# Kernel optimization log

Hardware: AMD Instinct MI355X
Metric: run time of the kernel (lower is better)

Reference implementation:

```python
import jax, jax.numpy as jnp
import numpy as np

D_MODEL = 2048
D_INNER = 4096            # expand * d_model
D_XB = 1024
D_STATE = 128
HEADDIM = 64
NHEADS = D_INNER // HEADDIM            # 64
NGROUPS = D_INNER // D_STATE           # 32 (d_inner == ngroups * d_state)
HPG = NHEADS // NGROUPS                # heads per B/C group = 2
REPEAT = D_INNER // D_XB               # repeat_kv factor = 4
XB_GROUPS = D_XB // D_STATE            # 8
CHUNK = 256
D_CONV = 4
CONV_DIM = D_INNER + 2 * D_XB          # 6144
D_IN_PROJ = D_INNER + 2 * D_XB + D_INNER + NHEADS  # 10304 -> d_mlp = 0
NORM_GS = D_INNER // NGROUPS           # gated group-RMSNorm group size = 128
EPS = 1e-5


def setup_inputs() -> dict:
    key = jax.random.key(0)
    ks = jax.random.split(key, 8)
    u = jax.random.normal(ks[0], (2, 2048, D_MODEL), jnp.float32)
    W_in = jax.random.normal(ks[1], (D_IN_PROJ, D_MODEL), jnp.float32) * 0.02
    conv_w = jax.random.normal(ks[2], (CONV_DIM, D_CONV), jnp.float32) * 0.2
    conv_b = jnp.zeros((CONV_DIM,), jnp.float32)
    # dt_bias = inverse-softplus of dt ~ LogUniform(dt_min, dt_max), as in __init__
    dt = jnp.exp(jax.random.uniform(ks[3], (NHEADS,), jnp.float32)
                 * (np.log(0.1) - np.log(0.001)) + np.log(0.001))
    dt_bias = dt + jnp.log(-jnp.expm1(-dt))
    A_log = jnp.log(jax.random.uniform(ks[4], (NHEADS,), jnp.float32, minval=1.0, maxval=16.0))
    D = jnp.ones((NHEADS,), jnp.float32)
    norm_weight = jnp.ones((D_INNER,), jnp.float32)
    W_out = jax.random.normal(ks[5], (D_MODEL, D_INNER), jnp.float32) * 0.02
    return dict(u=u, W_in=W_in, conv_w=conv_w, conv_b=conv_b, dt_bias=dt_bias,
                A_log=A_log, D=D, norm_weight=norm_weight, W_out=W_out)


def _segsum(x):
    # x: (..., T); out[..., t, s] = sum_{s < i <= t} x_i for s <= t else -inf
    T = x.shape[-1]
    cs = jnp.cumsum(x, axis=-1)
    seg = cs[..., :, None] - cs[..., None, :]
    mask = jnp.tril(jnp.ones((T, T), bool))
    return jnp.where(mask, seg, -jnp.inf)


def _chunked_scan(x, dt, A, Bh, Ch, D):
    # SSD chunked selective scan (mamba_chunk_scan_combined math).
    # x: (b,l,h,p), dt: (b,l,h) post-softplus, A: (h,), Bh/Ch: (b,l,h,n), D: (h,)
    b, l, h, p = x.shape
    c = l // CHUNK
    xc = x.reshape(b, c, CHUNK, h, p)
    dtc = dt.reshape(b, c, CHUNK, h)
    Bc = Bh.reshape(b, c, CHUNK, h, D_STATE)
    Cc = Ch.reshape(b, c, CHUNK, h, D_STATE)
    dA = jnp.transpose(dtc * A, (0, 3, 1, 2))          # (b,h,c,cl)
    dA_cs = jnp.cumsum(dA, axis=-1)                     # (b,h,c,cl)
    L = jnp.exp(_segsum(dA))                            # (b,h,c,cl,cl), lower-tri decay
    xdt = xc * dtc[..., None]                           # (b,c,cl,h,p)
    # intra-chunk (diagonal block) output
    G = jnp.einsum('bclhn,bcshn->bhcls', Cc, Bc)
    Y_diag = jnp.einsum('bhcls,bcshp->bclhp', G * L, xdt)
    # per-chunk final states
    decay_states = jnp.exp(dA_cs[..., -1:] - dA_cs)     # (b,h,c,cl)
    states = jnp.einsum('bcshn,bhcs,bcshp->bchpn', Bc, decay_states, xdt)
    # inter-chunk recurrence
    chunk_decay = jnp.exp(dA_cs[..., -1])               # (b,h,c)
    states_t = jnp.moveaxis(states, 1, 0)               # (c,b,h,p,n)
    decay_t = jnp.moveaxis(chunk_decay, -1, 0)          # (c,b,h)
    def step(carry, inp):
        s, d = inp
        return carry * d[..., None, None] + s, carry
    _, prev = jax.lax.scan(step, jnp.zeros_like(states_t[0]), (states_t, decay_t))
    prev = jnp.moveaxis(prev, 0, 1)                     # (b,c,h,p,n) state entering each chunk
    Y_off = jnp.einsum('bclhn,bchpn,bhcl->bclhp', Cc, prev, jnp.exp(dA_cs))
    y = Y_diag + Y_off + xc * D[:, None]                # D skip uses raw x
    return y.reshape(b, l, h, p)


def reference(u, W_in, conv_w, conv_b, dt_bias, A_log, D, norm_weight, W_out):
    b, l, _ = u.shape
    zxbcdt = u @ W_in.T                                 # (b,l,10304); d_mlp == 0
    z, xBC, dt = jnp.split(zxbcdt, [D_INNER, D_INNER + CONV_DIM], axis=-1)
    # causal depthwise conv1d (kernel D_CONV) + SiLU (causal_conv1d_fn semantics)
    xp = jnp.pad(xBC, ((0, 0), (D_CONV - 1, 0), (0, 0)))
    conv = conv_b
    for k in range(D_CONV):
        conv = conv + xp[:, k:k + l, :] * conv_w[:, k]
    xBC = jax.nn.silu(conv)
    x, B, C = jnp.split(xBC, [D_XB, 2 * D_XB], axis=-1)
    # GQA-style repeat_kv (repeat_interleave over d_state-sized groups)
    x = jnp.repeat(x.reshape(b, l, XB_GROUPS, D_STATE), REPEAT, axis=2).reshape(b, l, D_INNER)
    B = jnp.repeat(B.reshape(b, l, XB_GROUPS, D_STATE), REPEAT, axis=2)   # (b,l,NGROUPS,n)
    C = C.reshape(b, l, NGROUPS, D_STATE)
    # broadcast groups to heads (head h uses group h // HPG)
    Bh = jnp.repeat(B, HPG, axis=2)
    Ch = jnp.repeat(C, HPG, axis=2)
    xh = x.reshape(b, l, NHEADS, HEADDIM)
    dt = jax.nn.softplus(dt + dt_bias)                  # dt_softplus=True
    A = -jnp.exp(A_log)
    y = _chunked_scan(xh, dt, A, Bh, Ch, D).reshape(b, l, D_INNER)
    # RMSNormGated (norm_before_gate=False): gate then grouped RMSNorm
    y = y * jax.nn.silu(z)
    yg = y.reshape(b, l, NGROUPS, NORM_GS)
    rstd = jax.lax.rsqrt(jnp.mean(yg * yg, axis=-1, keepdims=True) + EPS)
    y = (yg * rstd).reshape(b, l, D_INNER) * norm_weight
    return y @ W_out.T
```

## Files before the change

kernel.cpp:

```cpp
#include <hip/hip_runtime.h>
#include <cstdint>
#include <cstddef>

typedef unsigned int uint;
typedef unsigned short ushort;

typedef __bf16 bf16x8 __attribute__((ext_vector_type(8)));
typedef float f32x4 __attribute__((ext_vector_type(4)));

__device__ __forceinline__ float bflo(uint u) { return __uint_as_float(u << 16); }
__device__ __forceinline__ float bfhi(uint u) { return __uint_as_float(u & 0xffff0000u); }
__device__ __forceinline__ float bf2f(ushort s) { return __uint_as_float(((uint)s) << 16); }
__device__ __forceinline__ ushort f2bf(float f) {
    uint u = __float_as_uint(f);
    u += 0x7fffu + ((u >> 16) & 1u);
    return (ushort)(u >> 16);
}
__device__ __forceinline__ uint pk2(float lo, float hi) {
    return (uint)f2bf(lo) | ((uint)f2bf(hi) << 16);
}
__device__ __forceinline__ void unpack8(uint4 v, float* f) {
    f[0] = bflo(v.x); f[1] = bfhi(v.x); f[2] = bflo(v.y); f[3] = bfhi(v.y);
    f[4] = bflo(v.z); f[5] = bfhi(v.z); f[6] = bflo(v.w); f[7] = bfhi(v.w);
}

typedef __attribute__((address_space(1))) const unsigned int* as1_cuptr;
typedef __attribute__((address_space(3))) unsigned int* as3_uptr;
__device__ __forceinline__ void gload_lds16(const void* g, void* l) {
    __builtin_amdgcn_global_load_lds((as1_cuptr)g, (as3_uptr)l, 16, 0, 0);
}

#define LTOT 4096
#define DMODEL 2048
#define DINNER 4096
#define DSTATE 128
#define NHEADS 64
#define CONVDIM 6144
#define DPROJ 10304
#define CHUNK 256
#define NCHUNK 16

__global__ void cvt_kernel(const float* __restrict__ in, ushort* __restrict__ out, int n4) {
    int i = blockIdx.x * 256 + threadIdx.x;
    if (i < n4) {
        float4 v = ((const float4*)in)[i];
        ushort4 o;
        o.x = f2bf(v.x); o.y = f2bf(v.y); o.z = f2bf(v.z); o.w = f2bf(v.w);
        ((ushort4*)out)[i] = o;
    }
}

#define MFMA_OP __builtin_amdgcn_mfma_f32_16x16x32_bf16
#define MM16(MB) do { \
  acc[(MB)+0][0]=MFMA_OP(a0,b0,acc[(MB)+0][0],0,0,0); acc[(MB)+0][1]=MFMA_OP(a0,b1,acc[(MB)+0][1],0,0,0); \
  acc[(MB)+0][2]=MFMA_OP(a0,b2,acc[(MB)+0][2],0,0,0); acc[(MB)+0][3]=MFMA_OP(a0,b3,acc[(MB)+0][3],0,0,0); \
  acc[(MB)+1][0]=MFMA_OP(a1,b0,acc[(MB)+1][0],0,0,0); acc[(MB)+1][1]=MFMA_OP(a1,b1,acc[(MB)+1][1],0,0,0); \
  acc[(MB)+1][2]=MFMA_OP(a1,b2,acc[(MB)+1][2],0,0,0); acc[(MB)+1][3]=MFMA_OP(a1,b3,acc[(MB)+1][3],0,0,0); \
  acc[(MB)+2][0]=MFMA_OP(a2,b0,acc[(MB)+2][0],0,0,0); acc[(MB)+2][1]=MFMA_OP(a2,b1,acc[(MB)+2][1],0,0,0); \
  acc[(MB)+2][2]=MFMA_OP(a2,b2,acc[(MB)+2][2],0,0,0); acc[(MB)+2][3]=MFMA_OP(a2,b3,acc[(MB)+2][3],0,0,0); \
  acc[(MB)+3][0]=MFMA_OP(a3,b0,acc[(MB)+3][0],0,0,0); acc[(MB)+3][1]=MFMA_OP(a3,b1,acc[(MB)+3][1],0,0,0); \
  acc[(MB)+3][2]=MFMA_OP(a3,b2,acc[(MB)+3][2],0,0,0); acc[(MB)+3][3]=MFMA_OP(a3,b3,acc[(MB)+3][3],0,0,0); \
} while (0)

#define RD8(BASE, OFF) (*(const bf16x8*)((BASE) + (OFF)))

__global__ __launch_bounds__(512, 2) void gemm256_in(
    const ushort* __restrict__ X, const ushort* __restrict__ W,
    ushort* __restrict__ zbuf, ushort* __restrict__ xbc, float* __restrict__ dtraw) {
    __shared__ ushort AL[2][16384];
    __shared__ ushort BL[2][16384];
    const int NBN = 41;
    int q = gridDim.x >> 3;
    int wg = blockIdx.x;
    int swz = (wg & 7) * q + (wg >> 3);
    int per = NBN * 4;
    int sg = swz / per, rr = swz % per;
    int bm = sg * 4 + (rr & 3);
    int bn = rr >> 2;
    int tid = threadIdx.x;
    int lane = tid & 63, w = tid >> 6;
    int wr = w >> 2, wc = w & 3;
    int lr = lane & 15, g = lane >> 4;
    int y00 = ((lr >> 1) << 7) | ((lr & 1) << 6) | (g << 4);
    int z00 = y00 ^ (((y00 >> 7) & 7) << 4);
    int aBase = wr * 8192 + z00;
    int bBase = wc * 4096 + z00;
    int z0 = tid * 16, z1 = z0 + 8192;
    int y0 = z0 ^ (((z0 >> 7) & 7) << 4);
    int y1 = z1 ^ (((z1 >> 7) & 7) << 4);
    int row0s = ((y0 >> 7) << 1) | ((y0 >> 6) & 1), kbe0 = (y0 & 63) >> 1;
    int row1s = ((y1 >> 7) << 1) | ((y1 >> 6) & 1), kbe1 = (y1 & 63) >> 1;
    const ushort* gA0 = &X[(size_t)(bm * 256 + row0s) * 2048 + kbe0];
    const ushort* gA1 = &X[(size_t)(bm * 256 + row1s) * 2048 + kbe1];
    const ushort* gB0 = &W[(size_t)(bn * 256 + row0s) * 2048 + kbe0];
    const ushort* gB1 = &W[(size_t)(bn * 256 + row1s) * 2048 + kbe1];
    int wOff = w * 1024;

#define STAGE(DB, ARR, KP, P0, P1, KO) do { \
    gload_lds16((P0) + (KO) + (KP) * 32, (char*)(ARR) + (DB) * 32768 + (KP) * 16384 + wOff); \
    gload_lds16((P1) + (KO) + (KP) * 32, (char*)(ARR) + (DB) * 32768 + (KP) * 16384 + wOff + 8192); \
} while (0)

    f32x4 acc[8][4] = {};
    STAGE(0, AL, 0, gA0, gA1, 0);
    STAGE(0, BL, 0, gB0, gB1, 0);
    STAGE(0, AL, 1, gA0, gA1, 0);
    STAGE(0, BL, 1, gB0, gB1, 0);

    for (int t = 0; t < 32; ++t) {
        int buf = t & 1, nb = buf ^ 1;
        int ko = ((t + 1) & 31) * 64;
        const char* Ab = (const char*)AL + buf * 32768;
        const char* Bb = (const char*)BL + buf * 32768;
        bf16x8 a0, a1, a2, a3, b0, b1, b2, b3;
        asm volatile("s_waitcnt vmcnt(4)" ::: "memory");
        __builtin_amdgcn_s_barrier();
        __builtin_amdgcn_sched_barrier(0);
        b0 = RD8(Bb, bBase);        b1 = RD8(Bb, bBase + 1024);
        b2 = RD8(Bb, bBase + 2048); b3 = RD8(Bb, bBase + 3072);
        a0 = RD8(Ab, aBase);        a1 = RD8(Ab, aBase + 1024);
        a2 = RD8(Ab, aBase + 2048); a3 = RD8(Ab, aBase + 3072);
        STAGE(nb, AL, 0, gA0, gA1, ko);
        __builtin_amdgcn_s_setprio(1);
        MM16(0);
        __builtin_amdgcn_s_setprio(0);
        __builtin_amdgcn_sched_barrier(0);
        __builtin_amdgcn_s_barrier();
        __builtin_amdgcn_sched_barrier(0);
        a0 = RD8(Ab, aBase + 4096);        a1 = RD8(Ab, aBase + 4096 + 1024);
        a2 = RD8(Ab, aBase + 4096 + 2048); a3 = RD8(Ab, aBase + 4096 + 3072);
        STAGE(nb, BL, 0, gB0, gB1, ko);
        __builtin_amdgcn_s_setprio(1);
        MM16(4);
        __builtin_amdgcn_s_setprio(0);
        asm volatile("s_waitcnt vmcnt(4)" ::: "memory");
        __builtin_amdgcn_s_barrier();
        __builtin_amdgcn_sched_barrier(0);
        b0 = RD8(Bb, bBase + 16384);        b1 = RD8(Bb, bBase + 16384 + 1024);
        b2 = RD8(Bb, bBase + 16384 + 2048); b3 = RD8(Bb, bBase + 16384 + 3072);
        a0 = RD8(Ab, aBase + 16384);        a1 = RD8(Ab, aBase + 16384 + 1024);
        a2 = RD8(Ab, aBase + 16384 + 2048); a3 = RD8(Ab, aBase + 16384 + 3072);
        STAGE(nb, AL, 1, gA0, gA1, ko);
        __builtin_amdgcn_s_setprio(1);
        MM16(0);
        __builtin_amdgcn_s_setprio(0);
        __builtin_amdgcn_sched_barrier(0);
        __builtin_amdgcn_s_barrier();
        __builtin_amdgcn_sched_barrier(0);
        a0 = RD8(Ab, aBase + 16384 + 4096);        a1 = RD8(Ab, aBase + 16384 + 4096 + 1024);
        a2 = RD8(Ab, aBase + 16384 + 4096 + 2048); a3 = RD8(Ab, aBase + 16384 + 4096 + 3072);
        STAGE(nb, BL, 1, gB0, gB1, ko);
        __builtin_amdgcn_s_setprio(1);
        MM16(4);
        __builtin_amdgcn_s_setprio(0);
    }
    asm volatile("s_waitcnt vmcnt(0)" ::: "memory");

    int rq = g * 4;
    #pragma unroll
    for (int mf = 0; mf < 8; mf++) {
        int row0 = bm * 256 + wr * 128 + mf * 16 + rq;
        #pragma unroll
        for (int n = 0; n < 4; n++) {
            int cb0 = bn * 256 + wc * 64 + n * 16;
            int col = cb0 + lr;
            if (cb0 < 4096) {
                #pragma unroll
                for (int r = 0; r < 4; r++)
                    zbuf[(size_t)(row0 + r) * DINNER + col] = f2bf(acc[mf][n][r]);
            } else if (cb0 < 10240) {
                #pragma unroll
                for (int r = 0; r < 4; r++)
                    xbc[(size_t)(row0 + r) * CONVDIM + (col - 4096)] = f2bf(acc[mf][n][r]);
            } else if (cb0 < 10304) {
                #pragma unroll
                for (int r = 0; r < 4; r++)
                    dtraw[(size_t)(row0 + r) * 64 + (col - 10240)] = acc[mf][n][r];
            }
        }
    }
}
#undef STAGE

__global__ __launch_bounds__(256) void gemm_bf16_out(
    const ushort* __restrict__ X, const ushort* __restrict__ W,
    float* __restrict__ outF, int M, int N, int K, int NB) {
    __shared__ ushort As[128 * 32];
    __shared__ ushort Bs[128 * 32];
    int q = gridDim.x >> 3;
    int wg = blockIdx.x;
    int swz = (wg & 7) * q + (wg >> 3);
    int per = NB * 4;
    int sg = swz / per, rr = swz % per;
    int bm = sg * 4 + (rr & 3);
    int bn = rr >> 2;
    int tid = threadIdx.x;
    int lane = tid & 63, w = tid >> 6;
    int wr = w >> 1, wc = w & 1;
    int lr = lane & 15, lk = (lane >> 4) * 8;
    int r0 = lane >> 2;
    int ce = (lane & 3) * 8;
    const ushort* gA0 = &X[(size_t)(bm * 128 + (w * 2 + 0) * 16 + r0) * K + ce];
    const ushort* gA1 = &X[(size_t)(bm * 128 + (w * 2 + 1) * 16 + r0) * K + ce];
    const ushort* gB0 = &W[(size_t)(bn * 128 + (w * 2 + 0) * 16 + r0) * K + ce];
    const ushort* gB1 = &W[(size_t)(bn * 128 + (w * 2 + 1) * 16 + r0) * K + ce];
    ushort* lA0 = &As[(w * 2 + 0) * 512];
    ushort* lA1 = &As[(w * 2 + 1) * 512];
    ushort* lB0 = &Bs[(w * 2 + 0) * 512];
    ushort* lB1 = &Bs[(w * 2 + 1) * 512];
    f32x4 acc[4][4] = {};
    for (int kk = 0; kk < K; kk += 32) {
        __syncthreads();
        gload_lds16(gA0, lA0); gload_lds16(gA1, lA1);
        gload_lds16(gB0, lB0); gload_lds16(gB1, lB1);
        gA0 += 32; gA1 += 32; gB0 += 32; gB1 += 32;
        __syncthreads();
        bf16x8 af[4], bfr[4];
        #pragma unroll
        for (int m = 0; m < 4; m++) af[m] = *(const bf16x8*)&As[(wr * 64 + m * 16 + lr) * 32 + lk];
        #pragma unroll
        for (int n = 0; n < 4; n++) bfr[n] = *(const bf16x8*)&Bs[(wc * 64 + n * 16 + lr) * 32 + lk];
        #pragma unroll
        for (int m = 0; m < 4; m++)
            #pragma unroll
            for (int n = 0; n < 4; n++)
                acc[m][n] = MFMA_OP(af[m], bfr[n], acc[m][n], 0, 0, 0);
    }
    int rq = (lane >> 4) * 4;
    #pragma unroll
    for (int m = 0; m < 4; m++) {
        int row0 = bm * 128 + wr * 64 + m * 16 + rq;
        #pragma unroll
        for (int n = 0; n < 4; n++) {
            int col = bn * 128 + wc * 64 + n * 16 + lr;
            #pragma unroll
            for (int r = 0; r < 4; r++)
                outF[(size_t)(row0 + r) * N + col] = acc[m][n][r];
        }
    }
}

__global__ void conv_kernel(const ushort* __restrict__ xbc, const float* __restrict__ cw,
                            const float* __restrict__ cb, ushort* __restrict__ convout) {
    int c8 = (blockIdx.x * 256 + threadIdx.x) * 8;
    int row0 = blockIdx.y * 4;
    int t0 = row0 & 2047;
    float bias[8];
    {
        float4 b0 = ((const float4*)cb)[c8 / 4];
        float4 b1 = ((const float4*)cb)[c8 / 4 + 1];
        bias[0] = b0.x; bias[1] = b0.y; bias[2] = b0.z; bias[3] = b0.w;
        bias[4] = b1.x; bias[5] = b1.y; bias[6] = b1.z; bias[7] = b1.w;
    }
    float wk[8][4];
    #pragma unroll
    for (int e = 0; e < 8; e++) {
        float4 wv = ((const float4*)cw)[c8 + e];
        wk[e][0] = wv.x; wk[e][1] = wv.y; wk[e][2] = wv.z; wk[e][3] = wv.w;
    }
    float f[7][8];
    #pragma unroll
    for (int j = 0; j < 7; j++) {
        int tt = t0 - 3 + j;
        if (tt >= 0) {
            uint4 v = *(const uint4*)&xbc[(size_t)(row0 - 3 + j) * CONVDIM + c8];
            unpack8(v, f[j]);
        } else {
            #pragma unroll
            for (int e = 0; e < 8; e++) f[j][e] = 0.f;
        }
    }
    #pragma unroll
    for (int r = 0; r < 4; r++) {
        float a[8];
        #pragma unroll
        for (int e = 0; e < 8; e++) {
            a[e] = bias[e];
            #pragma unroll
            for (int k = 0; k < 4; k++) a[e] += f[r + k][e] * wk[e][k];
        }
        uint4 o;
        float s[8];
        #pragma unroll
        for (int e = 0; e < 8; e++) s[e] = a[e] / (1.f + __expf(-a[e]));
        o.x = pk2(s[0], s[1]); o.y = pk2(s[2], s[3]);
        o.z = pk2(s[4], s[5]); o.w = pk2(s[6], s[7]);
        *(uint4*)&convout[(size_t)(row0 + r) * CONVDIM + c8] = o;
    }
}

__global__ void cumsum_kernel(float* __restrict__ dtbuf, const float* __restrict__ dt_bias,
                              const float* __restrict__ A_log, float* __restrict__ dAcs) {
    int bi = blockIdx.x;
    int h = bi & 63, cg = bi >> 6;
    int t = threadIdx.x;
    size_t didx = (size_t)(cg * 256 + t) * 64 + h;
    float x = dtbuf[didx] + dt_bias[h];
    float sp = (x > 20.f) ? x : log1pf(__expf(x));
    dtbuf[didx] = sp;
    float A = -expf(A_log[h]);
    float v = sp * A;
    __shared__ float s[256];
    s[t] = v;
    __syncthreads();
    for (int off = 1; off < 256; off <<= 1) {
        float add = (t >= off) ? s[t - off] : 0.f;
        __syncthreads();
        s[t] += add;
        __syncthreads();
    }
    dAcs[(size_t)bi * 256 + t] = s[t];
}

__global__ __launch_bounds__(256) void states_mfma(
    const ushort* __restrict__ convout, const float* __restrict__ dtsp,
    const float* __restrict__ dAcs, float* __restrict__ states) {
    __shared__ ushort BT[128 * 72];
    __shared__ ushort XT[64 * 72];
    int bi = blockIdx.x;
    int h = bi & 63, cg = bi >> 6;
    int tid = threadIdx.x;
    int rowbase = cg * 256;
    int bcol = 1024 + ((h >> 3) << 7);
    int xcol = ((h >> 3) << 7) + ((h & 1) << 6);
    float dAlast = dAcs[(size_t)bi * 256 + 255];
    int w = tid >> 6, lane = tid & 63, g = lane >> 4, cc = lane & 15;
    f32x4 acc[4][2] = {};
    for (int T = 0; T < 4; T++) {
        __syncthreads();
        int s = lane;
        int srow = rowbase + T * 64 + s;
        #pragma unroll
        for (int i = 0; i < 4; i++) {
            int n0 = (w + i * 4) * 8;
            uint4 v = *(const uint4*)&convout[(size_t)srow * CONVDIM + bcol + n0];
            ushort us[8];
            us[0] = (ushort)v.x; us[1] = (ushort)(v.x >> 16);
            us[2] = (ushort)v.y; us[3] = (ushort)(v.y >> 16);
            us[4] = (ushort)v.z; us[5] = (ushort)(v.z >> 16);
            us[6] = (ushort)v.w; us[7] = (ushort)(v.w >> 16);
            #pragma unroll
            for (int e = 0; e < 8; e++) BT[(n0 + e) * 72 + s] = us[e];
        }
        float wgt = dtsp[(size_t)srow * 64 + h] * __expf(dAlast - dAcs[(size_t)bi * 256 + T * 64 + s]);
        #pragma unroll
        for (int j = 0; j < 2; j++) {
            int p0 = (w * 2 + j) * 8;
            uint4 v = *(const uint4*)&convout[(size_t)srow * CONVDIM + xcol + p0];
            float f[8]; unpack8(v, f);
            #pragma unroll
            for (int e = 0; e < 8; e++) XT[(p0 + e) * 72 + s] = f2bf(f[e] * wgt);
        }
        __syncthreads();
        bf16x8 af[4][2], bw[2][2];
        #pragma unroll
        for (int m = 0; m < 4; m++)
            #pragma unroll
            for (int kb = 0; kb < 2; kb++)
                af[m][kb] = *(const bf16x8*)&XT[(m * 16 + cc) * 72 + kb * 32 + 8 * g];
        #pragma unroll
        for (int np = 0; np < 2; np++)
            #pragma unroll
            for (int kb = 0; kb < 2; kb++)
                bw[np][kb] = *(const bf16x8*)&BT[(w * 32 + np * 16 + cc) * 72 + kb * 32 + 8 * g];
        #pragma unroll
        for (int m = 0; m < 4; m++)
            #pragma unroll
            for (int np = 0; np < 2; np++) {
                acc[m][np] = MFMA_OP(af[m][0], bw[np][0], acc[m][np], 0, 0, 0);
                acc[m][np] = MFMA_OP(af[m][1], bw[np][1], acc[m][np], 0, 0, 0);
            }
    }
    size_t base = (size_t)bi * 8192;
    #pragma unroll
    for (int m = 0; m < 4; m++)
        #pragma unroll
        for (int np = 0; np < 2; np++)
            #pragma unroll
            for (int r = 0; r < 4; r++) {
                int p = m * 16 + 4 * g + r;
                int n = w * 32 + np * 16 + cc;
                states[base + (size_t)p * 128 + n] = acc[m][np][r];
            }
}

__global__ void recur_kernel(const float* __restrict__ dAcs, float* __restrict__ states) {
    int blk = blockIdx.x;
    int pq = blk & 7, bh = blk >> 3;
    int h = bh & 63, b = bh >> 6;
    int tid = threadIdx.x;
    int p = pq * 8 + (tid >> 5);
    int n0 = (tid & 31) * 4;
    float4 carry = make_float4(0.f, 0.f, 0.f, 0.f);
    for (int c = 0; c < 8; c++) {
        int bi = (b * 8 + c) * 64 + h;
        float decay = __expf(dAcs[(size_t)bi * 256 + 255]);
        size_t idx = (size_t)bi * 8192 + (size_t)p * 128 + n0;
        float4 tmp = *(const float4*)&states[idx];
        *(float4*)&states[idx] = carry;
        carry.x = carry.x * decay + tmp.x;
        carry.y = carry.y * decay + tmp.y;
        carry.z = carry.z * decay + tmp.z;
        carry.w = carry.w * decay + tmp.w;
    }
}

__global__ __launch_bounds__(256, 2) void yscan_mfma(
    const ushort* __restrict__ convout, const float* __restrict__ dtsp,
    const float* __restrict__ dAcs, const float* __restrict__ states,
    ushort* __restrict__ y) {
    __shared__ ushort XT[64 * 264];
    __shared__ ushort PR[64 * 136];
    __shared__ ushort PV[4 * 16 * 72];
    __shared__ float sdA[256];
    int bi = blockIdx.x;
    int h = bi & 63, cg = bi >> 6;
    int tid = threadIdx.x;
    int rowbase = cg * 256;
    int bcol = 1024 + ((h >> 3) << 7);
    int ccol = 2048 + ((h >> 1) << 7);
    int xcol = ((h >> 3) << 7) + ((h & 1) << 6);

    sdA[tid] = dAcs[(size_t)bi * 256 + tid];
    #pragma unroll
    for (int i = 0; i < 4; i++) {
        int s = i * 64 + (tid & 63);
        float dtv = dtsp[(size_t)(rowbase + s) * 64 + h];
        #pragma unroll
        for (int j = 0; j < 2; j++) {
            int p0 = (((tid >> 6) << 1) + j) << 3;
            uint4 v = *(const uint4*)&convout[(size_t)(rowbase + s) * CONVDIM + xcol + p0];
            float f[8]; unpack8(v, f);
            #pragma unroll
            for (int e = 0; e < 8; e++) XT[(p0 + e) * 264 + s] = f2bf(f[e] * dtv);
        }
    }
    {
        const float* pv = &states[(size_t)bi * 8192];
        #pragma unroll
        for (int i = 0; i < 8; i++) {
            int flat = i * 1024 + tid * 4;
            float4 v = *(const float4*)&pv[flat];
            int p = flat >> 7, n = flat & 127;
            *(uint*)&PR[p * 136 + n]     = pk2(v.x, v.y);
            *(uint*)&PR[p * 136 + n + 2] = pk2(v.z, v.w);
        }
    }
    __syncthreads();

    int w = tid >> 6, lane = tid & 63, g = lane >> 4, c = lane & 15;
    int wbase = w * 64;
    const ushort* Crow0 = &convout[(size_t)(rowbase + wbase + c) * CONVDIM + ccol + 8 * g];

    f32x4 yac[4][4] = {};
    #pragma unroll
    for (int kb = 0; kb < 4; kb++) {
        bf16x8 pb[4];
        #pragma unroll
        for (int np = 0; np < 4; np++)
            pb[np] = *(const bf16x8*)&PR[(16 * np + c) * 136 + kb * 32 + 8 * g];
        #pragma unroll
        for (int m = 0; m < 4; m++) {
            bf16x8 cf = *(const bf16x8*)&Crow0[(size_t)(m * 16) * CONVDIM + kb * 32];
            #pragma unroll
            for (int np = 0; np < 4; np++)
                yac[m][np] = MFMA_OP(cf, pb[np], yac[m][np], 0, 0, 0);
        }
    }
    float al[4][4];
    float Sw = sdA[wbase];
    float eSw = __expf(Sw);
    #pragma unroll
    for (int m = 0; m < 4; m++)
        #pragma unroll
        for (int r = 0; r < 4; r++) {
            float dAl = sdA[wbase + m * 16 + 4 * g + r];
            al[m][r] = __expf(dAl - Sw);
            float el = al[m][r] * eSw;
            #pragma unroll
            for (int np = 0; np < 4; np++) yac[m][np][r] *= el;
        }

    ushort* pvs = &PV[w * 1152];
    for (int T = 0; T <= w; T++) {
        f32x4 sac[4][4] = {};
        #pragma unroll
        for (int kb = 0; kb < 4; kb++) {
            bf16x8 bb[4];
            #pragma unroll
            for (int np = 0; np < 4; np++)
                bb[np] = *(const bf16x8*)&convout[(size_t)(rowbase + T * 64 + 16 * np + c) * CONVDIM + bcol + kb * 32 + 8 * g];
            #pragma unroll
            for (int m = 0; m < 4; m++) {
                bf16x8 cf = *(const bf16x8*)&Crow0[(size_t)(m * 16) * CONVDIM + kb * 32];
                #pragma unroll
                for (int np = 0; np < 4; np++)
                    sac[m][np] = MFMA_OP(cf, bb[np], sac[m][np], 0, 0, 0);
            }
        }
        bf16x8 xb[4][2];
        #pragma unroll
        for (int np = 0; np < 4; np++)
            #pragma unroll
            for (int k2 = 0; k2 < 2; k2++)
                xb[np][k2] = *(const bf16x8*)&XT[(16 * np + c) * 264 + T * 64 + k2 * 32 + 8 * g];
        if (T < w) {
            float ET = sdA[T * 64 + 63];
            float cT = __expf(Sw - ET);
            float bc[4];
            #pragma unroll
            for (int np = 0; np < 4; np++)
                bc[np] = __expf(ET - sdA[T * 64 + 16 * np + c]) * cT;
            #pragma unroll
            for (int m = 0; m < 4; m++) {
                #pragma unroll
                for (int np = 0; np < 4; np++) {
                    float s0 = bc[np];
                    #pragma unroll
                    for (int r = 0; r < 4; r++)
                        pvs[(4 * g + r) * 72 + 16 * np + c] = f2bf(sac[m][np][r] * (al[m][r] * s0));
                }
                bf16x8 pa0 = *(const bf16x8*)&pvs[c * 72 + 8 * g];
                bf16x8 pa1 = *(const bf16x8*)&pvs[c * 72 + 32 + 8 * g];
                #pragma unroll
                for (int np = 0; np < 4; np++) {
                    yac[m][np] = MFMA_OP(pa0, xb[np][0], yac[m][np], 0, 0, 0);
                    yac[m][np] = MFMA_OP(pa1, xb[np][1], yac[m][np], 0, 0, 0);
                }
            }
        } else {
            #pragma unroll
            for (int m = 0; m < 4; m++) {
                float dal[4];
                #pragma unroll
                for (int r = 0; r < 4; r++) dal[r] = sdA[wbase + m * 16 + 4 * g + r];
                #pragma unroll
                for (int np = 0; np < 4; np++) {
                    int s_loc = w * 64 + 16 * np + c;
                    float dAs = sdA[s_loc];
                    #pragma unroll
                    for (int r = 0; r < 4; r++) {
                        int l_loc = wbase + m * 16 + 4 * g + r;
                        float v = (s_loc <= l_loc) ? sac[m][np][r] * __expf(dal[r] - dAs) : 0.f;
                        pvs[(4 * g + r) * 72 + 16 * np + c] = f2bf(v);
                    }
                }
                bf16x8 pa0 = *(const bf16x8*)&pvs[c * 72 + 8 * g];
                bf16x8 pa1 = *(const bf16x8*)&pvs[c * 72 + 32 + 8 * g];
                #pragma unroll
                for (int np = 0; np < 4; np++) {
                    yac[m][np] = MFMA_OP(pa0, xb[np][0], yac[m][np], 0, 0, 0);
                    yac[m][np] = MFMA_OP(pa1, xb[np][1], yac[m][np], 0, 0, 0);
                }
            }
        }
    }
    #pragma unroll
    for (int m = 0; m < 4; m++)
        #pragma unroll
        for (int np = 0; np < 4; np++)
            #pragma unroll
            for (int r = 0; r < 4; r++) {
                int l = wbase + m * 16 + 4 * g + r;
                y[(size_t)(rowbase + l) * DINNER + h * 64 + 16 * np + c] = f2bf(yac[m][np][r]);
            }
}

__global__ void norm_kernel(ushort* __restrict__ y, const ushort* __restrict__ zbuf,
                            const ushort* __restrict__ convout, const float* __restrict__ Dvec,
                            const float* __restrict__ nw) {
    int row = blockIdx.x;
    int g = blockIdx.y * 4 + (threadIdx.x >> 6);
    int lane = threadIdx.x & 63;
    int cbase = g * 128 + lane * 2;
    int h = cbase >> 6;
    int p = cbase & 63;
    int xc = ((h >> 3) << 7) + ((h & 1) << 6) + p;
    uint yv = *(const uint*)&y[(size_t)row * DINNER + cbase];
    uint zv = *(const uint*)&zbuf[(size_t)row * DINNER + cbase];
    uint xv = *(const uint*)&convout[(size_t)row * CONVDIM + xc];
    float Dh = Dvec[h];
    float y0 = bflo(yv) + Dh * bflo(xv), y1 = bfhi(yv) + Dh * bfhi(xv);
    float z0 = bflo(zv), z1 = bfhi(zv);
    float v0 = y0 * (z0 / (1.f + __expf(-z0)));
    float v1 = y1 * (z1 / (1.f + __expf(-z1)));
    float ss = v0 * v0 + v1 * v1;
    #pragma unroll
    for (int off = 32; off; off >>= 1) ss += __shfl_xor(ss, off, 64);
    float rstd = rsqrtf(ss * (1.f / 128.f) + 1e-5f);
    v0 *= rstd * nw[cbase];
    v1 *= rstd * nw[cbase + 1];
    *(uint*)&y[(size_t)row * DINNER + cbase] = pk2(v0, v1);
}

extern "C" void kernel_launch(void* const* d_in, const int* in_sizes, int n_in,
                              void* d_out, int out_size, void* d_ws, size_t ws_size,
                              hipStream_t stream) {
    const float* u       = (const float*)d_in[0];
    const float* W_in    = (const float*)d_in[1];
    const float* conv_w  = (const float*)d_in[2];
    const float* conv_b  = (const float*)d_in[3];
    const float* dt_bias = (const float*)d_in[4];
    const float* A_log   = (const float*)d_in[5];
    const float* Dvec    = (const float*)d_in[6];
    const float* nw      = (const float*)d_in[7];
    const float* W_out   = (const float*)d_in[8];

    char* ws = (char*)d_ws;
    size_t off = 0;
    auto alloc = [&](size_t bytes) { void* p = ws + off; off += (bytes + 255) & ~(size_t)255; return p; };
    ushort* zbuf    = (ushort*)alloc((size_t)LTOT * DINNER * 2);
    void*   shreg   = alloc((size_t)LTOT * CONVDIM * 2);
    ushort* xbc     = (ushort*)shreg;
    float*  states  = (float*)shreg;
    ushort* Wout_bf = (ushort*)shreg;
    float*  dtbuf   = (float*) alloc((size_t)LTOT * 64 * 4);
    void*   convreg = alloc((size_t)LTOT * CONVDIM * 2);
    ushort* Win_bf  = (ushort*)convreg;
    ushort* convout = (ushort*)convreg;
    float*  dAcs    = (float*) alloc((size_t)1024 * 256 * 4);
    void*   ybreg   = alloc((size_t)LTOT * DINNER * 2);
    ushort* u_bf    = (ushort*)ybreg;
    ushort* ybuf    = (ushort*)ybreg;

    cvt_kernel<<<dim3(8192),  dim3(256), 0, stream>>>(u, u_bf, 2097152);
    cvt_kernel<<<dim3(20608), dim3(256), 0, stream>>>(W_in, Win_bf, 5275648);
    gemm256_in<<<dim3(656), dim3(512), 0, stream>>>(u_bf, Win_bf, zbuf, xbc, dtbuf);
    conv_kernel<<<dim3(3, 1024), dim3(256), 0, stream>>>(xbc, conv_w, conv_b, convout);
    cumsum_kernel<<<dim3(1024), dim3(256), 0, stream>>>(dtbuf, dt_bias, A_log, dAcs);
    states_mfma<<<dim3(1024), dim3(256), 0, stream>>>(convout, dtbuf, dAcs, states);
    recur_kernel<<<dim3(1024), dim3(256), 0, stream>>>(dAcs, states);
    yscan_mfma<<<dim3(1024), dim3(256), 0, stream>>>(convout, dtbuf, dAcs, states, ybuf);
    cvt_kernel<<<dim3(8192), dim3(256), 0, stream>>>(W_out, Wout_bf, 2097152);
    norm_kernel<<<dim3(4096, 8), dim3(256), 0, stream>>>(ybuf, zbuf, convout, Dvec, nw);
    gemm_bf16_out<<<dim3(512), dim3(256), 0, stream>>>(
        ybuf, Wout_bf, (float*)d_out, LTOT, DMODEL, DINNER, 16);
}
```

Baseline: 518.6 us.

## Rewrite output GEMM with 256x128 tiles, double-buffered LDS and swizzled layout

Replaces the simple single-buffered 128x128 output-projection GEMM with a 512-thread, 256x128-tile kernel. It reuses the input-projection GEMM's structure: a double-buffered, XOR-swizzled LDS layout, async global-to-LDS prefetch of the next k-slice overlapped with MFMA work, and explicit waitcnt/barrier/priority scheduling. The aim is to hide global load latency, avoid LDS bank conflicts and raise arithmetic intensity per block. In exchange the grid shrinks to 256 blocks and every dimension is hard-coded.

```diff
diff --git a/kernel.cpp b/kernel.cpp
--- a/kernel.cpp
+++ b/kernel.cpp
@@ -182,63 +182,95 @@
 }
 #undef STAGE
 
-__global__ __launch_bounds__(256) void gemm_bf16_out(
+__global__ __launch_bounds__(512, 2) void gemm256_out(
     const ushort* __restrict__ X, const ushort* __restrict__ W,
-    float* __restrict__ outF, int M, int N, int K, int NB) {
-    __shared__ ushort As[128 * 32];
-    __shared__ ushort Bs[128 * 32];
+    float* __restrict__ outF) {
+    __shared__ ushort AL[2][16384];
+    __shared__ ushort BL[2][8192];
     int q = gridDim.x >> 3;
     int wg = blockIdx.x;
     int swz = (wg & 7) * q + (wg >> 3);
-    int per = NB * 4;
+    int per = 16 * 4;
     int sg = swz / per, rr = swz % per;
     int bm = sg * 4 + (rr & 3);
     int bn = rr >> 2;
     int tid = threadIdx.x;
     int lane = tid & 63, w = tid >> 6;
     int wr = w >> 1, wc = w & 1;
-    int lr = lane & 15, lk = (lane >> 4) * 8;
-    int r0 = lane >> 2;
-    int ce = (lane & 3) * 8;
-    const ushort* gA0 = &X[(size_t)(bm * 128 + (w * 2 + 0) * 16 + r0) * K + ce];
-    const ushort* gA1 = &X[(size_t)(bm * 128 + (w * 2 + 1) * 16 + r0) * K + ce];
-    const ushort* gB0 = &W[(size_t)(bn * 128 + (w * 2 + 0) * 16 + r0) * K + ce];
-    const ushort* gB1 = &W[(size_t)(bn * 128 + (w * 2 + 1) * 16 + r0) * K + ce];
-    ushort* lA0 = &As[(w * 2 + 0) * 512];
-    ushort* lA1 = &As[(w * 2 + 1) * 512];
-    ushort* lB0 = &Bs[(w * 2 + 0) * 512];
-    ushort* lB1 = &Bs[(w * 2 + 1) * 512];
+    int lr = lane & 15, g = lane >> 4;
+    int y00 = ((lr >> 1) << 7) | ((lr & 1) << 6) | (g << 4);
+    int z00 = y00 ^ (((y00 >> 7) & 7) << 4);
+    int aBase = wr * 4096 + z00;
+    int bBase = wc * 4096 + z00;
+    int z0 = tid * 16, z1 = z0 + 8192;
+    int y0 = z0 ^ (((z0 >> 7) & 7) << 4);
+    int y1 = z1 ^ (((z1 >> 7) & 7) << 4);
+    int rowA0 = ((y0 >> 7) << 1) | ((y0 >> 6) & 1), kA0 = (y0 & 63) >> 1;
+    int rowA1 = ((y1 >> 7) << 1) | ((y1 >> 6) & 1), kA1 = (y1 & 63) >> 1;
+    const ushort* gA0 = &X[(size_t)(bm * 256 + rowA0) * 4096 + kA0];
+    const ushort* gA1 = &X[(size_t)(bm * 256 + rowA1) * 4096 + kA1];
+    const ushort* gB  = &W[(size_t)(bn * 128 + rowA0) * 4096 + kA0];
+    int wOff = w * 1024;
+
+#define STAGEA(DB, KP, KO) do { \
+    gload_lds16(gA0 + (KO) + (KP) * 32, (char*)AL + (DB) * 32768 + (KP) * 16384 + wOff); \
+    gload_lds16(gA1 + (KO) + (KP) * 32, (char*)AL + (DB) * 32768 + (KP) * 16384 + wOff + 8192); \
+} while (0)
+#define STAGEB(DB, KP, KO) \
+    gload_lds16(gB + (KO) + (KP) * 32, (char*)BL + (DB) * 16384 + (KP) * 8192 + wOff)
+
     f32x4 acc[4][4] = {};
-    for (int kk = 0; kk < K; kk += 32) {
-        __syncthreads();
-        gload_lds16(gA0, lA0); gload_lds16(gA1, lA1);
-        gload_lds16(gB0, lB0); gload_lds16(gB1, lB1);
-        gA0 += 32; gA1 += 32; gB0 += 32; gB1 += 32;
-        __syncthreads();
-        bf16x8 af[4], bfr[4];
-        #pragma unroll
-        for (int m = 0; m < 4; m++) af[m] = *(const bf16x8*)&As[(wr * 64 + m * 16 + lr) * 32 + lk];
-        #pragma unroll
-        for (int n = 0; n < 4; n++) bfr[n] = *(const bf16x8*)&Bs[(wc * 64 + n * 16 + lr) * 32 + lk];
-        #pragma unroll
-        for (int m = 0; m < 4; m++)
-            #pragma unroll
-            for (int n = 0; n < 4; n++)
-                acc[m][n] = MFMA_OP(af[m], bfr[n], acc[m][n], 0, 0, 0);
-    }
-    int rq = (lane >> 4) * 4;
-    #pragma unroll
-    for (int m = 0; m < 4; m++) {
-        int row0 = bm * 128 + wr * 64 + m * 16 + rq;
-        #pragma unroll
-        for (int n = 0; n < 4; n++) {
-            int col = bn * 128 + wc * 64 + n * 16 + lr;
+    STAGEA(0, 0, 0); STAGEB(0, 0, 0);
+    STAGEA(0, 1, 0); STAGEB(0, 1, 0);
+
+    for (int t = 0; t < 64; ++t) {
+        int buf = t & 1, nb = buf ^ 1;
+        int ko = ((t + 1) & 63) * 64;
+        const char* Ab = (const char*)AL + buf * 32768;
+        const char* Bb = (const char*)BL + buf * 16384;
+        bf16x8 a0, a1, a2, a3, b0, b1, b2, b3;
+        asm volatile("s_waitcnt vmcnt(3)" ::: "memory");
+        __builtin_amdgcn_s_barrier();
+        __builtin_amdgcn_sched_barrier(0);
+        b0 = RD8(Bb, bBase);        b1 = RD8(Bb, bBase + 1024);
+        b2 = RD8(Bb, bBase + 2048); b3 = RD8(Bb, bBase + 3072);
+        a0 = RD8(Ab, aBase);        a1 = RD8(Ab, aBase + 1024);
+        a2 = RD8(Ab, aBase + 2048); a3 = RD8(Ab, aBase + 3072);
+        STAGEA(nb, 0, ko); STAGEB(nb, 0, ko);
+        __builtin_amdgcn_s_setprio(1);
+        MM16(0);
+        __builtin_amdgcn_s_setprio(0);
+        __builtin_amdgcn_sched_barrier(0);
+        asm volatile("s_waitcnt vmcnt(3)" ::: "memory");
+        __builtin_amdgcn_s_barrier();
+        __builtin_amdgcn_sched_barrier(0);
+        b0 = RD8(Bb, bBase + 8192);        b1 = RD8(Bb, bBase + 8192 + 1024);
+        b2 = RD8(Bb, bBase + 8192 + 2048); b3 = RD8(Bb, bBase + 8192 + 3072);
+        a0 = RD8(Ab, aBase + 16384);        a1 = RD8(Ab, aBase + 16384 + 1024);
+        a2 = RD8(Ab, aBase + 16384 + 2048); a3 = RD8(Ab, aBase + 16384 + 3072);
+        STAGEA(nb, 1, ko); STAGEB(nb, 1, ko);
+        __builtin_amdgcn_s_setprio(1);
+        MM16(0);
+        __builtin_amdgcn_s_setprio(0);
+        __builtin_amdgcn_sched_barrier(0);
+    }
+    asm volatile("s_waitcnt vmcnt(0)" ::: "memory");
+
+    int rq = g * 4;
+    #pragma unroll
+    for (int mf = 0; mf < 4; mf++) {
+        int row0 = bm * 256 + wr * 64 + mf * 16 + rq;
+        #pragma unroll
+        for (int nf = 0; nf < 4; nf++) {
+            int col = bn * 128 + wc * 64 + nf * 16 + lr;
             #pragma unroll
             for (int r = 0; r < 4; r++)
-                outF[(size_t)(row0 + r) * N + col] = acc[m][n][r];
-        }
-    }
-}
+                outF[(size_t)(row0 + r) * DMODEL + col] = acc[mf][nf][r];
+        }
+    }
+}
+#undef STAGEA
+#undef STAGEB
 
 __global__ void conv_kernel(const ushort* __restrict__ xbc, const float* __restrict__ cw,
                             const float* __restrict__ cb, ushort* __restrict__ convout) {
@@ -633,6 +665,5 @@
     yscan_mfma<<<dim3(1024), dim3(256), 0, stream>>>(convout, dtbuf, dAcs, states, ybuf);
     cvt_kernel<<<dim3(8192), dim3(256), 0, stream>>>(W_out, Wout_bf, 2097152);
     norm_kernel<<<dim3(4096, 8), dim3(256), 0, stream>>>(ybuf, zbuf, convout, Dvec, nw);
-    gemm_bf16_out<<<dim3(512), dim3(256), 0, stream>>>(
-        ybuf, Wout_bf, (float*)d_out, LTOT, DMODEL, DINNER, 16);
-}
+    gemm256_out<<<dim3(256), dim3(512), 0, stream>>>(ybuf, Wout_bf, (float*)d_out);
+}
```

Result: faster. 498.7 us (-3.8%).
